# Kernel optimization log

Measured on AMD Instinct MI355X. Metric: run time of the kernel, lower is better.

The kernel has to match this reference:

```python
import jax, jax.numpy as jnp
import numpy as np

B = 1048576
L = 32

def setup_inputs() -> dict:
    key = jax.random.key(0)
    k1, k2 = jax.random.split(key)
    D_pred_logit = jax.random.normal(k1, (B, L), dtype=jnp.float32)
    # D is a true distribution over L bins: random positives normalized per row
    raw = jax.random.uniform(k2, (B, L), dtype=jnp.float32)
    D = raw / jnp.sum(raw, axis=1, keepdims=True)
    return {"D_pred_logit": D_pred_logit, "D": D}

def reference(D_pred_logit, D):
    Lc = D.shape[1]
    # Ordinal similarity matrix A[j,k] = 1 - |j-k|/(L-1)  (PSD by construction)
    idx = jnp.arange(Lc, dtype=jnp.float32)
    A = 1.0 - jnp.abs(idx[:, None] - idx[None, :]) / (Lc - 1)
    A = A.astype(D.dtype)
    Q = D - jax.nn.softmax(D_pred_logit, axis=1)  # [B, L]
    # mean(diag(Q @ A @ Q^T)) == mean over rows of sum((Q @ A) * Q, axis=1)
    # (same math; avoids the B x B intermediate of the original)
    per_row = jnp.sum((Q @ A) * Q, axis=1)  # [B]
    return jnp.mean(per_row)
```

## Files before the change

kernel.cpp:

```cpp
#include <hip/hip_runtime.h>


#define L_BINS  32
#define NTHREAD 256
#define PAD     36
#define NBLOCKS 1024

typedef float vfloat4 __attribute__((ext_vector_type(4)));

__device__ __forceinline__ vfloat4 nt_load4(const float* p) {
    return __builtin_nontemporal_load((const vfloat4*)p);
}

__global__ __launch_bounds__(NTHREAD) void qfd2_main(const float* __restrict__ logit,
                                                     const float* __restrict__ D,
                                                     float* __restrict__ partial,
                                                     int ntiles) {
    __shared__ float zbuf[NTHREAD * PAD];
    __shared__ float dbuf[NTHREAD * PAD];

    const int t = threadIdx.x;
    float acc = 0.0f;

    vfloat4 vz[8], vd[8];
    int g = blockIdx.x;

    if (g < ntiles) {
        const float* zg = logit + (size_t)g * (NTHREAD * L_BINS);
        const float* dg = D     + (size_t)g * (NTHREAD * L_BINS);
#pragma unroll
        for (int k = 0; k < 8; ++k) vz[k] = nt_load4(zg + (k * NTHREAD + t) * 4);
#pragma unroll
        for (int k = 0; k < 8; ++k) vd[k] = nt_load4(dg + (k * NTHREAD + t) * 4);
    }

    for (; g < ntiles; g += NBLOCKS) {
#pragma unroll
        for (int k = 0; k < 8; ++k) {
            const int p = k * NTHREAD + t;
            *(vfloat4*)&zbuf[(p >> 3) * PAD + (p & 7) * 4] = vz[k];
        }
#pragma unroll
        for (int k = 0; k < 8; ++k) {
            const int p = k * NTHREAD + t;
            *(vfloat4*)&dbuf[(p >> 3) * PAD + (p & 7) * 4] = vd[k];
        }
        __syncthreads();

        float z[L_BINS], d[L_BINS];
#pragma unroll
        for (int f = 0; f < 8; ++f) ((vfloat4*)z)[f] = *(const vfloat4*)&zbuf[t * PAD + f * 4];
#pragma unroll
        for (int f = 0; f < 8; ++f) ((vfloat4*)d)[f] = *(const vfloat4*)&dbuf[t * PAD + f * 4];
        __syncthreads();

        const int gn = g + NBLOCKS;
        if (gn < ntiles) {
            const float* zg = logit + (size_t)gn * (NTHREAD * L_BINS);
            const float* dg = D     + (size_t)gn * (NTHREAD * L_BINS);
#pragma unroll
            for (int k = 0; k < 8; ++k) vz[k] = nt_load4(zg + (k * NTHREAD + t) * 4);
#pragma unroll
            for (int k = 0; k < 8; ++k) vd[k] = nt_load4(dg + (k * NTHREAD + t) * 4);
        }

        float tm[16];
#pragma unroll
        for (int i = 0; i < 16; ++i) tm[i] = fmaxf(z[i], z[i + 16]);
#pragma unroll
        for (int i = 0; i < 8; ++i)  tm[i] = fmaxf(tm[i], tm[i + 8]);
#pragma unroll
        for (int i = 0; i < 4; ++i)  tm[i] = fmaxf(tm[i], tm[i + 4]);
        const float m = fmaxf(fmaxf(tm[0], tm[2]), fmaxf(tm[1], tm[3]));

#pragma unroll
        for (int i = 0; i < L_BINS; ++i) z[i] = __expf(z[i] - m);
        float u[16];
#pragma unroll
        for (int i = 0; i < 16; ++i) u[i] = z[i] + z[i + 16];
#pragma unroll
        for (int i = 0; i < 8; ++i)  u[i] = u[i] + u[i + 8];
#pragma unroll
        for (int i = 0; i < 4; ++i)  u[i] = u[i] + u[i + 4];
        const float rs = 1.0f / ((u[0] + u[2]) + (u[1] + u[3]));

        float P = 0.0f, sP = 0.0f, sP2 = 0.0f;
#pragma unroll
        for (int i = 0; i < L_BINS - 1; ++i) {
            P  += d[i] - z[i] * rs;
            sP += P;
            sP2 = fmaf(P, P, sP2);
        }
        P += d[L_BINS - 1] - z[L_BINS - 1] * rs;
        const float S = P;
        acc += (2.0f / 31.0f) * (sP2 - S * sP) + S * S;
    }

#pragma unroll
    for (int msk = 1; msk < 64; msk <<= 1) acc += __shfl_xor(acc, msk);

    __shared__ float wpart[NTHREAD / 64];
    if ((t & 63) == 0) wpart[t >> 6] = acc;
    __syncthreads();
    if (t == 0)
        partial[blockIdx.x] = (wpart[0] + wpart[1]) + (wpart[2] + wpart[3]);
}

__global__ __launch_bounds__(256) void qfd2_fin(const float* __restrict__ partial,
                                                float* __restrict__ out,
                                                int nblocks, int rows) {
    double a = 0.0;
    for (int i = threadIdx.x; i < nblocks; i += 256) a += (double)partial[i];
#pragma unroll
    for (int msk = 1; msk < 64; msk <<= 1) a += __shfl_xor(a, msk);

    __shared__ double wp[4];
    if ((threadIdx.x & 63) == 0) wp[threadIdx.x >> 6] = a;
    __syncthreads();
    if (threadIdx.x == 0)
        out[0] = (float)(((wp[0] + wp[1]) + (wp[2] + wp[3])) / (double)rows);
}

extern "C" void kernel_launch(void* const* d_in, const int* in_sizes, int n_in,
                              void* d_out, int out_size, void* d_ws, size_t ws_size,
                              hipStream_t stream) {
    const float* logit = (const float*)d_in[0];
    const float* D     = (const float*)d_in[1];
    float* out         = (float*)d_out;
    float* partial     = (float*)d_ws;

    const int rows   = in_sizes[0] / L_BINS;
    const int ntiles = rows / NTHREAD;

    qfd2_main<<<NBLOCKS, NTHREAD, 0, stream>>>(logit, D, partial, ntiles);
    qfd2_fin<<<1, 256, 0, stream>>>(partial, out, NBLOCKS, rows);
}
```

Baseline: 246.0 us.

## Split each row across 8 lanes with shuffle reductions instead of LDS transpose

Replaces the shared-memory transpose, where one thread owned a whole row, with an 8-lanes-per-row layout. Each lane loads one float4 and computes max, sum and prefix sums through sub-wavefront shuffles. This removes the LDS traffic and both block barriers per tile, and loads 8 rows per wave iteration for memory-level parallelism. In exchange it adds many shuffle instructions per row and drops the explicit register prefetch of the next tile.

```diff
diff --git a/kernel.cpp b/kernel.cpp
--- a/kernel.cpp
+++ b/kernel.cpp
@@ -3,8 +3,8 @@
 
 #define L_BINS  32
 #define NTHREAD 256
-#define PAD     36
 #define NBLOCKS 1024
+#define UNROLL  8
 
 typedef float vfloat4 __attribute__((ext_vector_type(4)));
 
@@ -15,85 +15,67 @@
 __global__ __launch_bounds__(NTHREAD) void qfd2_main(const float* __restrict__ logit,
                                                      const float* __restrict__ D,
                                                      float* __restrict__ partial,
-                                                     int ntiles) {
-    __shared__ float zbuf[NTHREAD * PAD];
-    __shared__ float dbuf[NTHREAD * PAD];
+                                                     int rows) {
+    const int t    = threadIdx.x;
+    const int lane = t & 63;
+    const int s    = lane & 7;
+    const int g    = lane >> 3;
+    const int wid  = blockIdx.x * (NTHREAD / 64) + (t >> 6);
+    const int nwaves = NBLOCKS * (NTHREAD / 64);
 
-    const int t = threadIdx.x;
+    const float w3 = (s == 7) ? 0.0f : 1.0f;
+
     float acc = 0.0f;
 
-    vfloat4 vz[8], vd[8];
-    int g = blockIdx.x;
-
-    if (g < ntiles) {
-        const float* zg = logit + (size_t)g * (NTHREAD * L_BINS);
-        const float* dg = D     + (size_t)g * (NTHREAD * L_BINS);
+    for (int base = wid * 64; base < rows; base += nwaves * 64) {
+        vfloat4 vz[UNROLL], vd[UNROLL];
 #pragma unroll
-        for (int k = 0; k < 8; ++k) vz[k] = nt_load4(zg + (k * NTHREAD + t) * 4);
-#pragma unroll
-        for (int k = 0; k < 8; ++k) vd[k] = nt_load4(dg + (k * NTHREAD + t) * 4);
-    }
-
-    for (; g < ntiles; g += NBLOCKS) {
-#pragma unroll
-        for (int k = 0; k < 8; ++k) {
-            const int p = k * NTHREAD + t;
-            *(vfloat4*)&zbuf[(p >> 3) * PAD + (p & 7) * 4] = vz[k];
-        }
-#pragma unroll
-        for (int k = 0; k < 8; ++k) {
-            const int p = k * NTHREAD + t;
-            *(vfloat4*)&dbuf[(p >> 3) * PAD + (p & 7) * 4] = vd[k];
-        }
-        __syncthreads();
-
-        float z[L_BINS], d[L_BINS];
-#pragma unroll
-        for (int f = 0; f < 8; ++f) ((vfloat4*)z)[f] = *(const vfloat4*)&zbuf[t * PAD + f * 4];
-#pragma unroll
-        for (int f = 0; f < 8; ++f) ((vfloat4*)d)[f] = *(const vfloat4*)&dbuf[t * PAD + f * 4];
-        __syncthreads();
-
-        const int gn = g + NBLOCKS;
-        if (gn < ntiles) {
-            const float* zg = logit + (size_t)gn * (NTHREAD * L_BINS);
-            const float* dg = D     + (size_t)gn * (NTHREAD * L_BINS);
-#pragma unroll
-            for (int k = 0; k < 8; ++k) vz[k] = nt_load4(zg + (k * NTHREAD + t) * 4);
-#pragma unroll
-            for (int k = 0; k < 8; ++k) vd[k] = nt_load4(dg + (k * NTHREAD + t) * 4);
+        for (int u = 0; u < UNROLL; ++u) {
+            int row = base + u * 8 + g;
+            int crow = row < rows ? row : rows - 1;
+            const size_t off = (size_t)crow * L_BINS + s * 4;
+            vz[u] = nt_load4(logit + off);
+            vd[u] = nt_load4(D + off);
         }
 
-        float tm[16];
 #pragma unroll
-        for (int i = 0; i < 16; ++i) tm[i] = fmaxf(z[i], z[i + 16]);
-#pragma unroll
-        for (int i = 0; i < 8; ++i)  tm[i] = fmaxf(tm[i], tm[i + 8]);
-#pragma unroll
-        for (int i = 0; i < 4; ++i)  tm[i] = fmaxf(tm[i], tm[i + 4]);
-        const float m = fmaxf(fmaxf(tm[0], tm[2]), fmaxf(tm[1], tm[3]));
+        for (int u = 0; u < UNROLL; ++u) {
+            const bool valid = (base + u * 8 + g) < rows;
+            const vfloat4 z = vz[u], d = vd[u];
 
-#pragma unroll
-        for (int i = 0; i < L_BINS; ++i) z[i] = __expf(z[i] - m);
-        float u[16];
-#pragma unroll
-        for (int i = 0; i < 16; ++i) u[i] = z[i] + z[i + 16];
-#pragma unroll
-        for (int i = 0; i < 8; ++i)  u[i] = u[i] + u[i + 8];
-#pragma unroll
-        for (int i = 0; i < 4; ++i)  u[i] = u[i] + u[i + 4];
-        const float rs = 1.0f / ((u[0] + u[2]) + (u[1] + u[3]));
+            float m = fmaxf(fmaxf(z.x, z.y), fmaxf(z.z, z.w));
+            m = fmaxf(m, __shfl_xor(m, 1, 8));
+            m = fmaxf(m, __shfl_xor(m, 2, 8));
+            m = fmaxf(m, __shfl_xor(m, 4, 8));
 
-        float P = 0.0f, sP = 0.0f, sP2 = 0.0f;
-#pragma unroll
-        for (int i = 0; i < L_BINS - 1; ++i) {
-            P  += d[i] - z[i] * rs;
-            sP += P;
-            sP2 = fmaf(P, P, sP2);
+            const float e0 = __expf(z.x - m), e1 = __expf(z.y - m);
+            const float e2 = __expf(z.z - m), e3 = __expf(z.w - m);
+            float sum = (e0 + e1) + (e2 + e3);
+            sum += __shfl_xor(sum, 1, 8);
+            sum += __shfl_xor(sum, 2, 8);
+            sum += __shfl_xor(sum, 4, 8);
+            const float rs = 1.0f / sum;
+
+            const float q0 = d.x - e0 * rs, q1 = d.y - e1 * rs;
+            const float q2 = d.z - e2 * rs, q3 = d.w - e3 * rs;
+            const float p0 = q0, p1 = p0 + q1, p2 = p1 + q2, p3 = p2 + q3;
+
+            const float T = p3;
+            float inc = T, tmp;
+            tmp = __shfl_up(inc, 1, 8); if (s >= 1) inc += tmp;
+            tmp = __shfl_up(inc, 2, 8); if (s >= 2) inc += tmp;
+            tmp = __shfl_up(inc, 4, 8); if (s >= 4) inc += tmp;
+            const float off_ = inc - T;
+            const float S    = __shfl(inc, 7, 8);
+
+            const float P0 = off_ + p0, P1 = off_ + p1;
+            const float P2 = off_ + p2, P3 = off_ + p3;
+
+            const float sPl  = ((P0 + P1) + P2) + w3 * P3;
+            const float sP2l = fmaf(P0, P0, fmaf(P1, P1, fmaf(P2, P2, w3 * P3 * P3)));
+            const float c    = (2.0f / 31.0f) * (sP2l - S * sPl) + 0.125f * (S * S);
+            acc += valid ? c : 0.0f;
         }
-        P += d[L_BINS - 1] - z[L_BINS - 1] * rs;
-        const float S = P;
-        acc += (2.0f / 31.0f) * (sP2 - S * sP) + S * S;
     }
 
 #pragma unroll
@@ -129,9 +111,8 @@
     float* out         = (float*)d_out;
     float* partial     = (float*)d_ws;
 
-    const int rows   = in_sizes[0] / L_BINS;
-    const int ntiles = rows / NTHREAD;
+    const int rows = in_sizes[0] / L_BINS;
 
-    qfd2_main<<<NBLOCKS, NTHREAD, 0, stream>>>(logit, D, partial, ntiles);
+    qfd2_main<<<NBLOCKS, NTHREAD, 0, stream>>>(logit, D, partial, rows);
     qfd2_fin<<<1, 256, 0, stream>>>(partial, out, NBLOCKS, rows);
 }
```

New measurement: 252.7 us. 1.03x slower.
